# Kernel optimization log

Hardware: AMD Instinct MI355X
Metric: run time of the kernel (lower is better)

Reference implementation:

```python
import math
import jax, jax.numpy as jnp
import numpy as np

B, S, D = 2, 1024, 4096
H, DH = 32, 128


def setup_inputs() -> dict:
    key = jax.random.key(0)
    ks = jax.random.split(key, 8)
    scale = 1.0 / math.sqrt(D)
    return {
        "hidden_q": jax.random.normal(ks[0], (B, S, D), jnp.float32),
        "hidden_kv": jax.random.normal(ks[1], (B, S, D), jnp.float32),
        "attention_mask": jax.random.randint(ks[2], (B, S, S), 0, 2) > 0,
        "position_bias": jax.random.normal(ks[3], (B, H, S, S), jnp.float32),
        "Wq": jax.random.normal(ks[4], (D, H * DH), jnp.float32) * scale,
        "Wk": jax.random.normal(ks[5], (D, H * DH), jnp.float32) * scale,
        "Wv": jax.random.normal(ks[6], (D, H * DH), jnp.float32) * scale,
        "Wo": jax.random.normal(ks[7], (H * DH, D), jnp.float32) * scale,
    }


def reference(hidden_q, hidden_kv, attention_mask, position_bias, Wq, Wk, Wv, Wo):
    b, len_q, _ = hidden_q.shape
    len_k = hidden_kv.shape[1]
    # projections -> [B, H, S, DH]
    q = (hidden_q @ Wq).reshape(b, len_q, H, DH).transpose(0, 2, 1, 3)
    k = (hidden_kv @ Wk).reshape(b, len_k, H, DH).transpose(0, 2, 1, 3)
    v = (hidden_kv @ Wv).reshape(b, len_k, H, DH).transpose(0, 2, 1, 3)
    # scores [B, H, Q, K]
    score = jnp.einsum("bhqd,bhkd->bhqk", q, k) / math.sqrt(DH)
    score = score + position_bias
    mask = attention_mask[:, None, :, :]  # [B,1,Q,K]
    score = jnp.where(mask, score, -jnp.inf)
    probs = jax.nn.softmax(score, axis=-1)
    probs = jnp.where(mask, probs, 0.0)  # post-softmax mask (also kills NaN rows)
    ctx = jnp.einsum("bhqk,bhkd->bhqd", probs, v)
    ctx = ctx.transpose(0, 2, 1, 3).reshape(b, len_q, H * DH)
    out = ctx @ Wo
    return out
```

## Files before the change

### kernel.cpp

```cpp
#include <hip/hip_runtime.h>
#include <stdint.h>


#define B_  2
#define S_  1024
#define D_  4096
#define H_  32
#define DH_ 128
#define M_  (B_ * S_)
#define KSTR 8192

typedef __attribute__((ext_vector_type(8))) short bf16x8;
typedef __attribute__((ext_vector_type(4))) float f32x4;

static __device__ __forceinline__ unsigned short f32_to_bf16(float f) {
    unsigned int x = __float_as_uint(f);
    x += 0x7fffu + ((x >> 16) & 1u);
    return (unsigned short)(x >> 16);
}

static __device__ __forceinline__ f32x4 mfma16(bf16x8 a, bf16x8 b, f32x4 c) {
    return __builtin_amdgcn_mfma_f32_16x16x32_bf16(a, b, c, 0, 0, 0);
}

#if defined(__has_builtin)
#if __has_builtin(__builtin_amdgcn_global_load_lds)
#define HAVE_GLOAD_LDS 1
#endif
#endif

#ifdef HAVE_GLOAD_LDS
#define GLD16(g, lbase, lane)                                                  \
    __builtin_amdgcn_global_load_lds(                                          \
        (const __attribute__((address_space(1))) void*)(g),                    \
        (__attribute__((address_space(3))) void*)(lbase), 16, 0, 0)
#else
#define GLD16(g, lbase, lane)                                                  \
    do { *(bf16x8*)((unsigned short*)(lbase) + (size_t)(lane) * 8) =           \
             *(const bf16x8*)(g); } while (0)
#endif

__global__ void detect_mask_kernel(const unsigned char* __restrict__ m, int* flag) {
    int l = threadIdx.x;
    uint4 v = ((const uint4*)m)[l];
    unsigned int ww[4] = {v.x, v.y, v.z, v.w};
    int nz_hi = 0, nz_lo01 = 0;
#pragma unroll
    for (int wi = 0; wi < 4; ++wi)
#pragma unroll
        for (int bi = 0; bi < 4; ++bi) {
            unsigned int byte = (ww[wi] >> (bi * 8)) & 0xffu;
            if (byte && bi != 0) nz_hi = 1;
            if (byte && bi <= 1) nz_lo01 = 1;
        }
    int any_hi = __any(nz_hi);
    int any_lo01 = __any(nz_lo01);
    if (l == 0) *flag = (!any_hi) ? 1 : ((!any_lo01) ? 2 : 0);
}

__global__ void canon_mask_kernel(const void* __restrict__ m, const int* __restrict__ flag,
                                  unsigned char* __restrict__ out, int n) {
    int i = blockIdx.x * 256 + threadIdx.x;
    if (i >= n) return;
    int f = *flag;
    unsigned char v;
    if (f == 1)      v = (unsigned char)(((const int*)m)[i] != 0);
    else if (f == 2) v = (unsigned char)(((const float*)m)[i] != 0.0f);
    else             v = (unsigned char)(((const unsigned char*)m)[i] != 0);
    out[i] = v;
}

__global__ void cvt2_bf16_kernel(const float* __restrict__ a, const float* __restrict__ b,
                                 unsigned short* __restrict__ oa, unsigned short* __restrict__ ob) {
    int i = blockIdx.x * 256 + threadIdx.x;
    const int n4 = (B_ * S_ * D_) / 4;
    const float* src = (i < n4) ? a : b;
    unsigned short* dst = (i < n4) ? oa : ob;
    int j = (i < n4) ? i : i - n4;
    float4 v = ((const float4*)src)[j];
    ushort4 o;
    o.x = f32_to_bf16(v.x); o.y = f32_to_bf16(v.y);
    o.z = f32_to_bf16(v.z); o.w = f32_to_bf16(v.w);
    ((ushort4*)dst)[j] = o;
}

__global__ __launch_bounds__(256) void transpose_all_kernel(
        const float* __restrict__ Wq, const float* __restrict__ Wk,
        const float* __restrict__ Wv, const float* __restrict__ Wo,
        unsigned short* __restrict__ WTq, unsigned short* __restrict__ WTkv,
        unsigned short* __restrict__ WTo) {
    __shared__ unsigned short lds[64][65];
    int which = blockIdx.x >> 12;
    int bid = blockIdx.x & 4095;
    const float* W = (which == 0) ? Wq : (which == 1) ? Wk : (which == 2) ? Wv : Wo;
    unsigned short* WT = (which == 0) ? WTq
                       : (which == 1) ? WTkv
                       : (which == 2) ? (WTkv + (size_t)4096 * 4096)
                                      : WTo;
    int bx = bid & 63;
    int by = bid >> 6;
    int t = threadIdx.x;
    int tr = t >> 4;
    int tc = (t & 15) * 4;
#pragma unroll
    for (int p = 0; p < 4; ++p) {
        int r = p * 16 + tr;
        float4 v = *(const float4*)(W + (size_t)(by * 64 + r) * D_ + bx * 64 + tc);
        lds[r][tc + 0] = f32_to_bf16(v.x);
        lds[r][tc + 1] = f32_to_bf16(v.y);
        lds[r][tc + 2] = f32_to_bf16(v.z);
        lds[r][tc + 3] = f32_to_bf16(v.w);
    }
    __syncthreads();
#pragma unroll
    for (int p = 0; p < 4; ++p) {
        int n = p * 16 + tr;
        ushort4 o;
        o.x = lds[tc + 0][n]; o.y = lds[tc + 1][n];
        o.z = lds[tc + 2][n]; o.w = lds[tc + 3][n];
        *(ushort4*)(WT + (size_t)(bx * 64 + n) * D_ + by * 64 + tc) = o;
    }
}

__global__ __launch_bounds__(256) void vt_kernel(const unsigned short* __restrict__ KV,
                                                 unsigned short* __restrict__ Vtw) {
    __shared__ unsigned short lds[64][72];
    int bid = blockIdx.x;
    int dt = bid & 1;
    int st = (bid >> 1) & 15;
    int h  = (bid >> 5) & 31;
    int b  = bid >> 10;
    int t = threadIdx.x;
    int r = t >> 2;
    int c0 = (t & 3) * 16;
    const unsigned short* src =
        KV + (size_t)(b * S_ + st * 64 + r) * KSTR + 4096 + h * DH_ + dt * 64 + c0;
    bf16x8 v0 = *(const bf16x8*)(src);
    bf16x8 v1 = *(const bf16x8*)(src + 8);
    *(bf16x8*)&lds[r][c0] = v0;
    *(bf16x8*)&lds[r][c0 + 8] = v1;
    __syncthreads();
    unsigned short tmp[16];
#pragma unroll
    for (int i = 0; i < 16; ++i) tmp[i] = lds[c0 + i][r];
    unsigned short* dst =
        Vtw + ((size_t)((b * H_ + h) * DH_ + dt * 64 + r)) * S_ + st * 64 + c0;
    *(bf16x8*)dst = *(bf16x8*)&tmp[0];
    *(bf16x8*)(dst + 8) = *(bf16x8*)&tmp[8];
}

template <int OUT_BF16>
__global__ __launch_bounds__(512, 2) void gemm8p_kernel(const unsigned short* __restrict__ A,
                                                        const unsigned short* __restrict__ BT,
                                                        void* __restrict__ C,
                                                        int M, int N, int K) {
    __shared__ unsigned short lds[3][24576];
    char* ldsc = (char*)&lds[0][0];

    int nbn = N >> 8;
    int bm = (int)blockIdx.x / nbn;
    int bn = (int)blockIdx.x % nbn;
    int m0 = bm << 7, n0 = bn << 8;
    int t = threadIdx.x, w = t >> 6, l = t & 63;
    int lr = l & 15, lg = l >> 4;
    int wm = (w >> 2) << 6;
    int wn = (w & 3) << 6;

    f32x4 acc[2][4];
    f32x4 ac[4][4];
    f32x4 vzero = {0.f, 0.f, 0.f, 0.f};
#pragma unroll
    for (int i = 0; i < 4; ++i)
#pragma unroll
        for (int j = 0; j < 4; ++j) ac[i][j] = vzero;
    (void)acc;

    int sch = (l & 7) ^ (l >> 3);
    int subrow = l >> 3;

#define STAGE(KT, BUF)                                                         \
    do { int koff_ = (KT) << 6;                                                \
        _Pragma("unroll")                                                      \
        for (int i = 0; i < 6; ++i) {                                          \
            int seg = w * 6 + i;                                               \
            char* dst = ldsc + (size_t)(BUF) * 49152 + (size_t)seg * 1024;     \
            if (seg < 16) {                                                    \
                int row = m0 + seg * 8 + subrow;                               \
                GLD16(A + (size_t)row * K + koff_ + (sch << 3), dst, l);       \
            } else {                                                           \
                int row = n0 + (seg - 16) * 8 + subrow;                        \
                GLD16(BT + (size_t)row * K + koff_ + (sch << 3), dst, l);      \
            }                                                                  \
        }                                                                      \
    } while (0)

    const int NT = K >> 6;
    STAGE(0, 0);
    STAGE(1, 1);

    int cur = 0;
    int pre = 2;
#pragma unroll 1
    for (int kt = 0; kt < NT; ++kt) {
        asm volatile("s_waitcnt lgkmcnt(0)" ::: "memory");
        __builtin_amdgcn_s_barrier();
        if (kt + 2 < NT) {
            STAGE(kt + 2, pre);
            asm volatile("s_waitcnt vmcnt(12)" ::: "memory");
        } else if (kt + 1 < NT) {
            asm volatile("s_waitcnt vmcnt(6)" ::: "memory");
        } else {
            asm volatile("s_waitcnt vmcnt(0)" ::: "memory");
        }
        __builtin_amdgcn_s_barrier();

        const char* Ab = ldsc + (size_t)cur * 49152;
        const char* Bb = Ab + 16384;

        bf16x8 bfr[4][2], af0[2][2], af1[2][2];
#pragma unroll
        for (int ni = 0; ni < 4; ++ni)
#pragma unroll
            for (int kk = 0; kk < 2; ++kk) {
                int row = wn + ni * 16 + lr;
                bfr[ni][kk] = *(const bf16x8*)(Bb + row * 128 +
                                ((((kk << 2) + lg) ^ (row & 7)) << 4));
            }
#pragma unroll
        for (int mi = 0; mi < 2; ++mi)
#pragma unroll
            for (int kk = 0; kk < 2; ++kk) {
                int row = wm + mi * 16 + lr;
                af0[mi][kk] = *(const bf16x8*)(Ab + row * 128 +
                                ((((kk << 2) + lg) ^ (row & 7)) << 4));
            }
        __builtin_amdgcn_s_setprio(1);
#pragma unroll
        for (int mi = 0; mi < 2; ++mi)
#pragma unroll
            for (int ni = 0; ni < 4; ++ni)
#pragma unroll
                for (int kk = 0; kk < 2; ++kk)
                    ac[mi][ni] = mfma16(af0[mi][kk], bfr[ni][kk], ac[mi][ni]);
        __builtin_amdgcn_s_setprio(0);
#pragma unroll
        for (int mi = 0; mi < 2; ++mi)
#pragma unroll
            for (int kk = 0; kk < 2; ++kk) {
                int row = wm + (mi + 2) * 16 + lr;
                af1[mi][kk] = *(const bf16x8*)(Ab + row * 128 +
                                ((((kk << 2) + lg) ^ (row & 7)) << 4));
            }
        __builtin_amdgcn_s_setprio(1);
#pragma unroll
        for (int mi = 0; mi < 2; ++mi)
#pragma unroll
            for (int ni = 0; ni < 4; ++ni)
#pragma unroll
                for (int kk = 0; kk < 2; ++kk)
                    ac[mi + 2][ni] = mfma16(af1[mi][kk], bfr[ni][kk], ac[mi + 2][ni]);
        __builtin_amdgcn_s_setprio(0);

        cur = (cur == 2) ? 0 : cur + 1;
        pre = (pre == 2) ? 0 : pre + 1;
    }
#undef STAGE

#pragma unroll
    for (int mi = 0; mi < 4; ++mi)
#pragma unroll
        for (int ni = 0; ni < 4; ++ni)
#pragma unroll
            for (int r = 0; r < 4; ++r) {
                int row = m0 + wm + mi * 16 + lg * 4 + r;
                int col = n0 + wn + ni * 16 + lr;
                if (OUT_BF16)
                    ((unsigned short*)C)[(size_t)row * N + col] = f32_to_bf16(ac[mi][ni][r]);
                else
                    ((float*)C)[(size_t)row * N + col] = ac[mi][ni][r];
            }
}

#define NEGF (-1e30f)
__global__ __launch_bounds__(256, 2) void attn_kernel(const unsigned short* __restrict__ Qw,
                                                      const unsigned short* __restrict__ KV,
                                                      const unsigned short* __restrict__ Vtw,
                                                      const float* __restrict__ bias,
                                                      const unsigned char* __restrict__ maskc,
                                                      unsigned short* __restrict__ ctx) {
    __shared__ unsigned short Kbuf[2][64 * 128];
    __shared__ unsigned short Vbuf[2][128 * 64];
    __shared__ unsigned short Plds[4][16 * 72];

    int bid = blockIdx.x;
    int qt = bid & 15, h = (bid >> 4) & 31, b = bid >> 9;
    int t = threadIdx.x, w = t >> 6, l = t & 63;
    int lr = l & 15, lg = l >> 4;
    int q0 = (qt << 6) + (w << 4);

    bf16x8 qf[4];
    const unsigned short* Qp = Qw + ((size_t)(b * S_ + q0 + lr)) * D_ + h * DH_ + lg * 8;
#pragma unroll
    for (int kf = 0; kf < 4; ++kf) qf[kf] = *(const bf16x8*)(Qp + kf * 32);

    f32x4 o[8];
    f32x4 vzero = {0.f, 0.f, 0.f, 0.f};
#pragma unroll
    for (int i = 0; i < 8; ++i) o[i] = vzero;
    float m_run[4], l_run[4];
#pragma unroll
    for (int r = 0; r < 4; ++r) { m_run[r] = NEGF; l_run[r] = 0.f; }

    const float* biasp = bias + (((size_t)(b * H_ + h)) << 20)
                              + (((size_t)(q0 + (lg << 2))) << 10) + lr;
    const unsigned char* mp = maskc + ((size_t)b << 20)
                              + (((size_t)(q0 + (lg << 2))) << 10) + lr;
    const unsigned short* Kg = KV + (size_t)(b * S_) * KSTR + h * DH_;
    const unsigned short* Vg = Vtw + (((size_t)(b * H_ + h)) * DH_) * S_;

    float br0[16], br1[16];
    int mr0[16], mr1[16];

#define STAGE_KV(KT, BUF)                                                          \
    do { int kv0_ = (KT) << 6;                                                     \
        _Pragma("unroll")                                                          \
        for (int c = 0; c < 4; ++c) {                                              \
            int seg = (w << 2) + c;                                                \
            int krow = (seg << 2) + (l >> 4);                                      \
            int kch = (l & 15) ^ (krow & 7);                                       \
            GLD16(Kg + (size_t)(kv0_ + krow) * KSTR + (kch << 3),                  \
                  &Kbuf[BUF][seg << 9], l);                                        \
            int vrow = (seg << 3) + (l >> 3);                                      \
            int vch = (l & 7) ^ (vrow & 7);                                        \
            GLD16(Vg + (size_t)vrow * S_ + kv0_ + (vch << 3),                      \
                  &Vbuf[BUF][seg << 9], l);                                        \
        }                                                                          \
    } while (0)

#define LOAD_BM(BR, MR, KT)                                                        \
    do { int kv0_ = (KT) << 6;                                                     \
        _Pragma("unroll")                                                          \
        for (int nb = 0; nb < 4; ++nb)                                             \
            _Pragma("unroll")                                                      \
            for (int r = 0; r < 4; ++r) {                                          \
                BR[nb * 4 + r] = biasp[((size_t)r << 10) + kv0_ + (nb << 4)];      \
                MR[nb * 4 + r] = mp[((size_t)r << 10) + kv0_ + (nb << 4)];         \
            }                                                                      \
    } while (0)

#define COMPUTE(BUF, BR, MR)                                                       \
    do {                                                                           \
        f32x4 s_[4];                                                               \
        _Pragma("unroll")                                                          \
        for (int nb = 0; nb < 4; ++nb) {                                           \
            s_[nb] = vzero;                                                        \
            int krow = (nb << 4) + lr;                                             \
            _Pragma("unroll")                                                      \
            for (int kf = 0; kf < 4; ++kf) {                                       \
                int ba = ((krow << 8) + (((kf << 5) + (lg << 3)) << 1))            \
                         ^ ((krow & 7) << 4);                                      \
                bf16x8 kfr = *(const bf16x8*)((const char*)Kbuf[BUF] + ba);        \
                s_[nb] = mfma16(qf[kf], kfr, s_[nb]);                              \
            }                                                                      \
        }                                                                          \
        float sv[4][4];                                                            \
        _Pragma("unroll")                                                          \
        for (int nb = 0; nb < 4; ++nb)                                             \
            _Pragma("unroll")                                                      \
            for (int r = 0; r < 4; ++r) {                                          \
                float x = fmaf(s_[nb][r], 0.08838834764831845f, BR[nb * 4 + r]);   \
                sv[nb][r] = MR[nb * 4 + r] ? x : NEGF;                             \
            }                                                                      \
        float mt[4], al[4], rs[4];                                                 \
        _Pragma("unroll")                                                          \
        for (int r = 0; r < 4; ++r)                                                \
            mt[r] = fmaxf(fmaxf(sv[0][r], sv[1][r]), fmaxf(sv[2][r], sv[3][r]));   \
        _Pragma("unroll")                                                          \
        for (int off = 1; off < 16; off <<= 1)                                     \
            _Pragma("unroll")                                                      \
            for (int r = 0; r < 4; ++r) mt[r] = fmaxf(mt[r], __shfl_xor(mt[r], off, 64)); \
        _Pragma("unroll")                                                          \
        for (int r = 0; r < 4; ++r) {                                              \
            float mn = fmaxf(m_run[r], mt[r]);                                     \
            al[r] = __expf(m_run[r] - mn);                                         \
            m_run[r] = mn;                                                         \
        }                                                                          \
        _Pragma("unroll")                                                          \
        for (int nb = 0; nb < 4; ++nb)                                             \
            _Pragma("unroll")                                                      \
            for (int r = 0; r < 4; ++r) sv[nb][r] = __expf(sv[nb][r] - m_run[r]);  \
        _Pragma("unroll")                                                          \
        for (int r = 0; r < 4; ++r)                                                \
            rs[r] = (sv[0][r] + sv[1][r]) + (sv[2][r] + sv[3][r]);                 \
        _Pragma("unroll")                                                          \
        for (int off = 1; off < 16; off <<= 1)                                     \
            _Pragma("unroll")                                                      \
            for (int r = 0; r < 4; ++r) rs[r] += __shfl_xor(rs[r], off, 64);       \
        _Pragma("unroll")                                                          \
        for (int r = 0; r < 4; ++r) l_run[r] = l_run[r] * al[r] + rs[r];           \
        _Pragma("unroll")                                                          \
        for (int nb2 = 0; nb2 < 8; ++nb2) {                                        \
            o[nb2][0] *= al[0]; o[nb2][1] *= al[1];                                \
            o[nb2][2] *= al[2]; o[nb2][3] *= al[3];                                \
        }                                                                          \
        _Pragma("unroll")                                                          \
        for (int nb = 0; nb < 4; ++nb)                                             \
            _Pragma("unroll")                                                      \
            for (int r = 0; r < 4; ++r)                                            \
                Plds[w][((lg << 2) + r) * 72 + (nb << 4) + lr] = f32_to_bf16(sv[nb][r]); \
        _Pragma("unroll")                                                          \
        for (int kf2 = 0; kf2 < 2; ++kf2) {                                        \
            bf16x8 pf = *(const bf16x8*)&Plds[w][lr * 72 + (kf2 << 5) + (lg << 3)]; \
            _Pragma("unroll")                                                      \
            for (int nb2 = 0; nb2 < 8; ++nb2) {                                    \
                int dh = (nb2 << 4) + lr;                                          \
                int ba = ((dh << 7) + (((kf2 << 5) + (lg << 3)) << 1))             \
                         ^ ((dh & 7) << 4);                                        \
                bf16x8 vf = *(const bf16x8*)((const char*)Vbuf[BUF] + ba);         \
                o[nb2] = mfma16(pf, vf, o[nb2]);                                   \
            }                                                                      \
        }                                                                          \
    } while (0)

    STAGE_KV(0, 0);
    LOAD_BM(br0, mr0, 0);

#pragma unroll 1
    for (int kt = 0; kt < 16; kt += 2) {
        __syncthreads();
        STAGE_KV(kt + 1, 1);
        LOAD_BM(br1, mr1, kt + 1);
        COMPUTE(0, br0, mr0);
        __syncthreads();
        if (kt < 14) {
            STAGE_KV(kt + 2, 0);
            LOAD_BM(br0, mr0, kt + 2);
        }
        COMPUTE(1, br1, mr1);
    }

#pragma unroll
    for (int r = 0; r < 4; ++r) {
        float inv = l_run[r] > 0.f ? 1.0f / l_run[r] : 0.f;
        int q = q0 + (lg << 2) + r;
        unsigned short* cp = ctx + ((size_t)(b * S_ + q)) * D_ + h * DH_ + lr;
#pragma unroll
        for (int nb2 = 0; nb2 < 8; ++nb2)
            cp[nb2 * 16] = f32_to_bf16(o[nb2][r] * inv);
    }
#undef STAGE_KV
#undef LOAD_BM
#undef COMPUTE
}

extern "C" void kernel_launch(void* const* d_in, const int* in_sizes, int n_in,
                              void* d_out, int out_size, void* d_ws, size_t ws_size,
                              hipStream_t stream) {
    const float* hq   = (const float*)d_in[0];
    const float* hkv  = (const float*)d_in[1];
    const void*  mask = d_in[2];
    const float* bias = (const float*)d_in[3];
    const float* Wq   = (const float*)d_in[4];
    const float* Wk   = (const float*)d_in[5];
    const float* Wv   = (const float*)d_in[6];
    const float* Wo   = (const float*)d_in[7];
    float* out = (float*)d_out;

    char* ws = (char*)d_ws;
    unsigned char* mask_c = (unsigned char*)ws;
    int* flag             = (int*)(ws + (2u << 20));
    unsigned short* hq_b  = (unsigned short*)(ws + (2u << 20) + 4096);
    unsigned short* hkv_b = hq_b + ((size_t)1 << 23);
    unsigned short* WTq   = hkv_b + ((size_t)1 << 23);
    unsigned short* WTo   = WTq + ((size_t)1 << 24);
    unsigned short* WTkv  = WTo + ((size_t)1 << 24);
    unsigned short* Qws   = WTkv + ((size_t)1 << 25);
    unsigned short* KVws  = Qws + ((size_t)1 << 23);
    unsigned short* Cws   = KVws + ((size_t)1 << 24);
    unsigned short* Vtw   = Cws + ((size_t)1 << 23);

    detect_mask_kernel<<<1, 64, 0, stream>>>((const unsigned char*)mask, flag);
    canon_mask_kernel<<<8192, 256, 0, stream>>>(mask, flag, mask_c, B_ * S_ * S_);
    cvt2_bf16_kernel<<<16384, 256, 0, stream>>>(hq, hkv, hq_b, hkv_b);
    transpose_all_kernel<<<16384, 256, 0, stream>>>(Wq, Wk, Wv, Wo, WTq, WTkv, WTo);

    gemm8p_kernel<1><<<(M_ / 128) * (D_ / 256), 512, 0, stream>>>(hq_b, WTq, Qws, M_, D_, D_);
    gemm8p_kernel<1><<<(M_ / 128) * (2 * D_ / 256), 512, 0, stream>>>(hkv_b, WTkv, KVws, M_, 2 * D_, D_);

    vt_kernel<<<B_ * H_ * 16 * 2, 256, 0, stream>>>(KVws, Vtw);
    attn_kernel<<<B_ * H_ * (S_ / 64), 256, 0, stream>>>(Qws, KVws, Vtw, bias, mask_c, Cws);

    gemm8p_kernel<0><<<(M_ / 128) * (D_ / 256), 512, 0, stream>>>(Cws, WTo, out, M_, D_, D_);
}
```

Baseline: 534.1 us.

## Rewrite GEMMs with 256x256 tiles, 9-slot pipeline, fused QKV launch, split-K output

Replaces the 128x256-tile GEMM with a 256x256-tile core that uses a 9-slot LDS ring of 16KB sub-tiles, issuing one load per quarter-step and sharing a barrier with the MFMA sub-steps. The Q and KV projections are merged into one 384-block launch with an XCD-aware block remap. The output projection becomes a 2-way split-K, writing fp32 partials that a separate kernel adds together. The larger tiles cut global traffic per FLOP and the merged launch removes tail effects, at the cost of more accumulator registers, an extra fp32 partial buffer and an extra reduction pass.

```diff
diff --git a/kernel.cpp b/kernel.cpp
--- a/kernel.cpp
+++ b/kernel.cpp
@@ -149,136 +149,157 @@
     *(bf16x8*)(dst + 8) = *(bf16x8*)&tmp[8];
 }
 
-template <int OUT_BF16>
-__global__ __launch_bounds__(512, 2) void gemm8p_kernel(const unsigned short* __restrict__ A,
-                                                        const unsigned short* __restrict__ BT,
-                                                        void* __restrict__ C,
-                                                        int M, int N, int K) {
-    __shared__ unsigned short lds[3][24576];
-    char* ldsc = (char*)&lds[0][0];
-
-    int nbn = N >> 8;
-    int bm = (int)blockIdx.x / nbn;
-    int bn = (int)blockIdx.x % nbn;
-    int m0 = bm << 7, n0 = bn << 8;
-    int t = threadIdx.x, w = t >> 6, l = t & 63;
-    int lr = l & 15, lg = l >> 4;
-    int wm = (w >> 2) << 6;
-    int wn = (w & 3) << 6;
-
-    f32x4 acc[2][4];
-    f32x4 ac[4][4];
+__device__ __forceinline__ void gemm_core(const unsigned short* __restrict__ A,
+                                          const unsigned short* __restrict__ BT,
+                                          void* __restrict__ C, int out_f32,
+                                          int m0, int n0, int cstride,
+                                          int koff, int NT, char* ldsc) {
+    const int t = threadIdx.x;
+    const int w = t >> 6, l = t & 63;
+    const int lr = l & 15, lg = l >> 4;
+    const int wmh = w >> 2;
+    const int walf = w & 3;
+    const int wm = wmh << 7;
+    const int wn = walf << 6;
+
+    const int ca0 = lg ^ (lr & 7);
+    const int aoff0 = lr * 128 + (ca0 << 4);
+    const int aoff1 = lr * 128 + ((ca0 ^ 4) << 4);
+    const int boff0 = ((walf & 1) * 64 + lr) * 128 + (ca0 << 4);
+    const int boff1 = ((walf & 1) * 64 + lr) * 128 + ((ca0 ^ 4) << 4);
+
+    const int srow = t >> 3;
+    const int sch = (t & 7) ^ (srow & 7);
+    const size_t soff0 = (size_t)srow * 4096 + (size_t)(sch << 3);
+    const size_t soff1 = soff0 + (size_t)64 * 4096;
+    const int ldso = w << 10;
+
+    f32x4 ac[8][4];
     f32x4 vzero = {0.f, 0.f, 0.f, 0.f};
 #pragma unroll
-    for (int i = 0; i < 4; ++i)
+    for (int i = 0; i < 8; ++i)
 #pragma unroll
         for (int j = 0; j < 4; ++j) ac[i][j] = vzero;
-    (void)acc;
-
-    int sch = (l & 7) ^ (l >> 3);
-    int subrow = l >> 3;
-
-#define STAGE(KT, BUF)                                                         \
-    do { int koff_ = (KT) << 6;                                                \
-        _Pragma("unroll")                                                      \
-        for (int i = 0; i < 6; ++i) {                                          \
-            int seg = w * 6 + i;                                               \
-            char* dst = ldsc + (size_t)(BUF) * 49152 + (size_t)seg * 1024;     \
-            if (seg < 16) {                                                    \
-                int row = m0 + seg * 8 + subrow;                               \
-                GLD16(A + (size_t)row * K + koff_ + (sch << 3), dst, l);       \
-            } else {                                                           \
-                int row = n0 + (seg - 16) * 8 + subrow;                        \
-                GLD16(BT + (size_t)row * K + koff_ + (sch << 3), dst, l);      \
-            }                                                                  \
-        }                                                                      \
+
+#define STAGE_ELEM(E, SS)                                                      \
+    do {                                                                       \
+        int er_ = (E) & 3;                                                     \
+        const unsigned short* mb_ = (er_ < 2)                                  \
+            ? A + (size_t)(m0 + ((er_ & 1) << 7)) * 4096                       \
+            : BT + (size_t)(n0 + ((er_ & 1) << 7)) * 4096;                     \
+        mb_ += (size_t)((((E) >> 2) << 6) + koff);                             \
+        char* d0_ = ldsc + (SS) * 16384 + ldso;                                \
+        GLD16(mb_ + soff0, d0_, l);                                            \
+        GLD16(mb_ + soff1, d0_ + 8192, l);                                     \
     } while (0)
 
-    const int NT = K >> 6;
-    STAGE(0, 0);
-    STAGE(1, 1);
-
-    int cur = 0;
-    int pre = 2;
+#pragma unroll
+    for (int e = 0; e < 5; ++e) STAGE_ELEM(e, e);
+
+    const int NT4 = NT << 2;
+    int E = 5, ss = 5, s0 = 0;
+    bf16x8 bfr[4][2];
+
 #pragma unroll 1
-    for (int kt = 0; kt < NT; ++kt) {
-        asm volatile("s_waitcnt lgkmcnt(0)" ::: "memory");
-        __builtin_amdgcn_s_barrier();
-        if (kt + 2 < NT) {
-            STAGE(kt + 2, pre);
-            asm volatile("s_waitcnt vmcnt(12)" ::: "memory");
-        } else if (kt + 1 < NT) {
-            asm volatile("s_waitcnt vmcnt(6)" ::: "memory");
-        } else {
-            asm volatile("s_waitcnt vmcnt(0)" ::: "memory");
+    for (int tau = 0; tau < NT; ++tau) {
+        int sA = s0 + wmh;          if (sA >= 9) sA -= 9;
+        int sB = s0 + 2 + (walf >> 1); if (sB >= 9) sB -= 9;
+        const char* pA0 = ldsc + sA * 16384 + aoff0;
+        const char* pA1 = ldsc + sA * 16384 + aoff1;
+        const char* pB0 = ldsc + sB * 16384 + boff0;
+        const char* pB1 = ldsc + sB * 16384 + boff1;
+#pragma unroll
+        for (int r = 0; r < 4; ++r) {
+            if (r == 0) {
+                if (tau == NT - 1)
+                    asm volatile("s_waitcnt vmcnt(0)" ::: "memory");
+                else
+                    asm volatile("s_waitcnt vmcnt(2)" ::: "memory");
+            }
+            __builtin_amdgcn_s_barrier();
+            asm volatile("" ::: "memory");
+            if (r == 0) {
+#pragma unroll
+                for (int nf = 0; nf < 4; ++nf) {
+                    bfr[nf][0] = *(const bf16x8*)(pB0 + nf * 2048);
+                    bfr[nf][1] = *(const bf16x8*)(pB1 + nf * 2048);
+                }
+            }
+            bf16x8 af[2][2];
+            int mfb = r << 1;
+#pragma unroll
+            for (int j = 0; j < 2; ++j) {
+                af[j][0] = *(const bf16x8*)(pA0 + (mfb + j) * 2048);
+                af[j][1] = *(const bf16x8*)(pA1 + (mfb + j) * 2048);
+            }
+            if (E < NT4) STAGE_ELEM(E, ss);
+            ++E; ss = (ss == 8) ? 0 : ss + 1;
+            __builtin_amdgcn_s_setprio(1);
+#pragma unroll
+            for (int j = 0; j < 2; ++j)
+#pragma unroll
+                for (int nf = 0; nf < 4; ++nf) {
+                    ac[mfb + j][nf] = mfma16(af[j][0], bfr[nf][0], ac[mfb + j][nf]);
+                    ac[mfb + j][nf] = mfma16(af[j][1], bfr[nf][1], ac[mfb + j][nf]);
+                }
+            __builtin_amdgcn_s_setprio(0);
         }
-        __builtin_amdgcn_s_barrier();
-
-        const char* Ab = ldsc + (size_t)cur * 49152;
-        const char* Bb = Ab + 16384;
-
-        bf16x8 bfr[4][2], af0[2][2], af1[2][2];
-#pragma unroll
-        for (int ni = 0; ni < 4; ++ni)
-#pragma unroll
-            for (int kk = 0; kk < 2; ++kk) {
-                int row = wn + ni * 16 + lr;
-                bfr[ni][kk] = *(const bf16x8*)(Bb + row * 128 +
-                                ((((kk << 2) + lg) ^ (row & 7)) << 4));
+        s0 += 4; if (s0 >= 9) s0 -= 9;
+    }
+#undef STAGE_ELEM
+
+#pragma unroll
+    for (int mf = 0; mf < 8; ++mf)
+#pragma unroll
+        for (int nf = 0; nf < 4; ++nf)
+#pragma unroll
+            for (int q = 0; q < 4; ++q) {
+                int row = m0 + wm + mf * 16 + lg * 4 + q;
+                int col = n0 + wn + nf * 16 + lr;
+                if (out_f32)
+                    ((float*)C)[(size_t)row * cstride + col] = ac[mf][nf][q];
+                else
+                    ((unsigned short*)C)[(size_t)row * cstride + col] = f32_to_bf16(ac[mf][nf][q]);
             }
-#pragma unroll
-        for (int mi = 0; mi < 2; ++mi)
-#pragma unroll
-            for (int kk = 0; kk < 2; ++kk) {
-                int row = wm + mi * 16 + lr;
-                af0[mi][kk] = *(const bf16x8*)(Ab + row * 128 +
-                                ((((kk << 2) + lg) ^ (row & 7)) << 4));
-            }
-        __builtin_amdgcn_s_setprio(1);
-#pragma unroll
-        for (int mi = 0; mi < 2; ++mi)
-#pragma unroll
-            for (int ni = 0; ni < 4; ++ni)
-#pragma unroll
-                for (int kk = 0; kk < 2; ++kk)
-                    ac[mi][ni] = mfma16(af0[mi][kk], bfr[ni][kk], ac[mi][ni]);
-        __builtin_amdgcn_s_setprio(0);
-#pragma unroll
-        for (int mi = 0; mi < 2; ++mi)
-#pragma unroll
-            for (int kk = 0; kk < 2; ++kk) {
-                int row = wm + (mi + 2) * 16 + lr;
-                af1[mi][kk] = *(const bf16x8*)(Ab + row * 128 +
-                                ((((kk << 2) + lg) ^ (row & 7)) << 4));
-            }
-        __builtin_amdgcn_s_setprio(1);
-#pragma unroll
-        for (int mi = 0; mi < 2; ++mi)
-#pragma unroll
-            for (int ni = 0; ni < 4; ++ni)
-#pragma unroll
-                for (int kk = 0; kk < 2; ++kk)
-                    ac[mi + 2][ni] = mfma16(af1[mi][kk], bfr[ni][kk], ac[mi + 2][ni]);
-        __builtin_amdgcn_s_setprio(0);
-
-        cur = (cur == 2) ? 0 : cur + 1;
-        pre = (pre == 2) ? 0 : pre + 1;
+}
+
+__global__ __launch_bounds__(512, 2) void gemm_qkv_kernel(
+        const unsigned short* __restrict__ Aq, const unsigned short* __restrict__ Bq,
+        unsigned short* __restrict__ Cq,
+        const unsigned short* __restrict__ Akv, const unsigned short* __restrict__ Bkv,
+        unsigned short* __restrict__ Ckv) {
+    __shared__ char ldsbuf[9 * 16384];
+    int bid = blockIdx.x;
+    int newid = (bid & 7) * 48 + (bid >> 3);
+    if (newid < 128) {
+        int bm = newid >> 4, bn = newid & 15;
+        gemm_core(Aq, Bq, Cq, 0, bm << 8, bn << 8, 4096, 0, 64, ldsbuf);
+    } else {
+        int e = newid - 128;
+        int bm = e >> 5, bn = e & 31;
+        gemm_core(Akv, Bkv, Ckv, 0, bm << 8, bn << 8, 8192, 0, 64, ldsbuf);
     }
-#undef STAGE
-
-#pragma unroll
-    for (int mi = 0; mi < 4; ++mi)
-#pragma unroll
-        for (int ni = 0; ni < 4; ++ni)
-#pragma unroll
-            for (int r = 0; r < 4; ++r) {
-                int row = m0 + wm + mi * 16 + lg * 4 + r;
-                int col = n0 + wn + ni * 16 + lr;
-                if (OUT_BF16)
-                    ((unsigned short*)C)[(size_t)row * N + col] = f32_to_bf16(ac[mi][ni][r]);
-                else
-                    ((float*)C)[(size_t)row * N + col] = ac[mi][ni][r];
-            }
+}
+
+__global__ __launch_bounds__(512, 2) void gemm_o_kernel(
+        const unsigned short* __restrict__ A, const unsigned short* __restrict__ BT,
+        float* __restrict__ P) {
+    __shared__ char ldsbuf[9 * 16384];
+    int bid = blockIdx.x;
+    int newid = (bid & 7) * 32 + (bid >> 3);
+    int ks = newid >> 7;
+    int tile = newid & 127;
+    int bm = tile >> 4, bn = tile & 15;
+    gemm_core(A, BT, P + (size_t)ks * M_ * D_, 1, bm << 8, bn << 8, 4096,
+              ks * 2048, 32, ldsbuf);
+}
+
+__global__ void reduce_o_kernel(const float* __restrict__ P, float* __restrict__ out) {
+    int i = blockIdx.x * 256 + threadIdx.x;
+    float4 a = ((const float4*)P)[i];
+    float4 b = ((const float4*)(P + (size_t)M_ * D_))[i];
+    float4 o; o.x = a.x + b.x; o.y = a.y + b.y; o.z = a.z + b.z; o.w = a.w + b.w;
+    ((float4*)out)[i] = o;
 }
 
 #define NEGF (-1e30f)
@@ -478,17 +499,18 @@
     unsigned short* KVws  = Qws + ((size_t)1 << 23);
     unsigned short* Cws   = KVws + ((size_t)1 << 24);
     unsigned short* Vtw   = Cws + ((size_t)1 << 23);
+    float* Pws            = (float*)(Vtw + ((size_t)1 << 23));
 
     detect_mask_kernel<<<1, 64, 0, stream>>>((const unsigned char*)mask, flag);
     canon_mask_kernel<<<8192, 256, 0, stream>>>(mask, flag, mask_c, B_ * S_ * S_);
     cvt2_bf16_kernel<<<16384, 256, 0, stream>>>(hq, hkv, hq_b, hkv_b);
     transpose_all_kernel<<<16384, 256, 0, stream>>>(Wq, Wk, Wv, Wo, WTq, WTkv, WTo);
 
-    gemm8p_kernel<1><<<(M_ / 128) * (D_ / 256), 512, 0, stream>>>(hq_b, WTq, Qws, M_, D_, D_);
-    gemm8p_kernel<1><<<(M_ / 128) * (2 * D_ / 256), 512, 0, stream>>>(hkv_b, WTkv, KVws, M_, 2 * D_, D_);
+    gemm_qkv_kernel<<<384, 512, 0, stream>>>(hq_b, WTq, Qws, hkv_b, WTkv, KVws);
 
     vt_kernel<<<B_ * H_ * 16 * 2, 256, 0, stream>>>(KVws, Vtw);
     attn_kernel<<<B_ * H_ * (S_ / 64), 256, 0, stream>>>(Qws, KVws, Vtw, bias, mask_c, Cws);
 
-    gemm8p_kernel<0><<<(M_ / 128) * (D_ / 256), 512, 0, stream>>>(Cws, WTo, out, M_, D_, D_);
-}
+    gemm_o_kernel<<<256, 512, 0, stream>>>(Cws, WTo, Pws);
+    reduce_o_kernel<<<(M_ * D_) / 1024, 256, 0, stream>>>(Pws, out);
+}
```

Result: no change. 526.3 us (-1.5%).
